# Kernel tuning notes

Measured on AMD Instinct MI355X. Metric: run time of the kernel, lower is better.

The kernel has to match this reference:

```python
import jax, jax.numpy as jnp
import numpy as np


def setup_inputs() -> dict:
    key = jax.random.key(0)
    ks = jax.random.split(key, 11)
    b, c, h, w = 16, 64, 16, 16
    F = 64  # num_filters
    O = 64  # num_outputs
    d_in = 2 * (c + 1)  # 130: concat of two (feature + coord) vectors
    s = 0.05
    return {
        "x_img": jax.random.normal(ks[0], (b, c, h, w), dtype=jnp.float32),
        "Wg0": jax.random.normal(ks[1], (F, d_in), dtype=jnp.float32) * s,
        "bg0": jax.random.normal(ks[2], (F,), dtype=jnp.float32) * s,
        "Wg1": jax.random.normal(ks[3], (F, F), dtype=jnp.float32) * s,
        "bg1": jax.random.normal(ks[4], (F,), dtype=jnp.float32) * s,
        "Wg2": jax.random.normal(ks[5], (F, F), dtype=jnp.float32) * s,
        "bg2": jax.random.normal(ks[6], (F,), dtype=jnp.float32) * s,
        "Wp": jax.random.normal(ks[7], (F, F), dtype=jnp.float32) * s,
        "bp": jax.random.normal(ks[8], (F,), dtype=jnp.float32) * s,
        "Wo": jax.random.normal(ks[9], (O, F), dtype=jnp.float32) * s,
        "bo": jax.random.normal(ks[10], (O,), dtype=jnp.float32) * s,
    }


def reference(x_img, Wg0, bg0, Wg1, bg1, Wg2, bg2, Wp, bp, Wo, bo):
    b, c, h, w = x_img.shape
    L = h * w
    # [b, L, c]: flatten spatial, move channels last
    feats = x_img.reshape(b, c, L).transpose(0, 2, 1)
    # append 1-d coordinate feature -> [b, L, c+1]
    coord = jnp.broadcast_to(
        jnp.arange(L, dtype=feats.dtype).reshape(1, L, 1), (b, L, 1)
    )
    feats = jnp.concatenate([feats, coord], axis=2)
    # pairwise broadcast-concat: pair[b, p, q] = [feats[b, q], feats[b, p]]
    d = feats.shape[-1]
    x_i = jnp.broadcast_to(feats[:, None, :, :], (b, L, L, d))
    x_j = jnp.broadcast_to(feats[:, :, None, :], (b, L, L, d))
    pair = jnp.concatenate([x_i, x_j], axis=3)  # [b, L, L, 2*(c+1)]
    # shared g-MLP (3 layers, ReLU)
    out = jax.nn.relu(jnp.einsum("bpqd,fd->bpqf", pair, Wg0) + bg0)
    out = jax.nn.relu(jnp.einsum("bpqf,gf->bpqg", out, Wg1) + bg1)
    out = jax.nn.relu(jnp.einsum("bpqf,gf->bpqg", out, Wg2) + bg2)
    # sum-reduce over both pair dims -> [b, F]
    out = out.sum(axis=(1, 2))
    # f-network
    out = jax.nn.relu(out @ Wp.T + bp)
    out = out @ Wo.T + bo
    return out
```

## Files before the change

### kernel.cpp

```cpp
#include <hip/hip_runtime.h>


typedef short s8v __attribute__((ext_vector_type(8)));
typedef short s4v __attribute__((ext_vector_type(4)));
typedef float f4v __attribute__((ext_vector_type(4)));

#define KEEP(x) asm volatile("" : "+v"(x))

#define MFMA16(a, b, c) __builtin_amdgcn_mfma_f32_16x16x16bf16_1k(a, b, c, 0, 0, 0)

__device__ __forceinline__ short bfr(float v) {
  return __builtin_bit_cast(short, (__bf16)v);
}
__device__ __forceinline__ f4v relu4(f4v v) {
  f4v z = {0.f, 0.f, 0.f, 0.f};
  return __builtin_elementwise_max(v, z);
}
__device__ __forceinline__ s8v cvt8(f4v a, f4v b) {
  s8v r;
  r[0] = bfr(a[0]); r[1] = bfr(a[1]); r[2] = bfr(a[2]); r[3] = bfr(a[3]);
  r[4] = bfr(b[0]); r[5] = bfr(b[1]); r[6] = bfr(b[2]); r[7] = bfr(b[3]);
  return r;
}
__device__ __forceinline__ s4v cvt4(f4v a) {
  s4v r;
  r[0] = bfr(a[0]); r[1] = bfr(a[1]); r[2] = bfr(a[2]); r[3] = bfr(a[3]);
  return r;
}
__device__ __forceinline__ f4v ldf4(const float* p) {
  return *(const f4v*)p;
}

__global__ __launch_bounds__(256) void k_pre(
    const float* __restrict__ x, const float* __restrict__ Wg0,
    const float* __restrict__ bg0, float* __restrict__ Ag,
    float* __restrict__ Bg) {
  __shared__ float ws[64 * 131];
  __shared__ float xs[64 * 17];

  const int t = threadIdx.x;
  const int b = blockIdx.x >> 4;
  const int l0 = (blockIdx.x & 15) * 16;

  for (int i = t; i < 64 * 130; i += 256) {
    int f = i / 130, d = i - f * 130;
    ws[f * 131 + d] = Wg0[i];
  }
  for (int i = t; i < 64 * 16; i += 256) {
    int ch = i >> 4, li = i & 15;
    xs[ch * 17 + li] = x[b * 16384 + ch * 256 + l0 + li];
  }
  __syncthreads();

  const int f = t & 63;
  const int w = t >> 6;
  float accA[4] = {0.f, 0.f, 0.f, 0.f};
  float accB[4] = {0.f, 0.f, 0.f, 0.f};
  for (int d = 0; d < 64; ++d) {
    float wa = ws[f * 131 + d];
    float wb = ws[f * 131 + 65 + d];
#pragma unroll
    for (int i = 0; i < 4; ++i) {
      float xv = xs[d * 17 + w + 4 * i];
      accA[i] += xv * wa;
      accB[i] += xv * wb;
    }
  }
  const float wca = ws[f * 131 + 64];
  const float wcb = ws[f * 131 + 129];
  const float bias = bg0[f];
#pragma unroll
  for (int i = 0; i < 4; ++i) {
    int l = l0 + w + 4 * i;
    Ag[(b * 256 + l) * 64 + f] = accA[i] + (float)l * wca;
    Bg[(b * 256 + l) * 64 + f] = accB[i] + (float)l * wcb + bias;
  }
}

__global__ __launch_bounds__(256, 1) void k_main(
    const float* __restrict__ Ag, const float* __restrict__ Bg,
    const float* __restrict__ Wg1, const float* __restrict__ bg1,
    const float* __restrict__ Wg2, const float* __restrict__ bg2,
    float* __restrict__ Part) {
  __shared__ __align__(16) float Bs[32 * 64];
  __shared__ float Sblk[64];

  const int t = threadIdx.x;
  const int wid = t >> 6;
  const int lane = t & 63;
  const int mm = lane & 15;
  const int quad = lane >> 4;
  const int b = blockIdx.y;
  const int blkx = blockIdx.x;
  const int qq = blkx & 3;
  const int p0 = (blkx >> 2) * 32;
  const int q0 = (qq * 4 + wid) * 16;

  if (t < 64) Sblk[t] = 0.f;

  {
    const f4v* Bb4 = (const f4v*)(Bg + (b * 256 + p0) * 64);
    ((f4v*)Bs)[t] = Bb4[t];
    ((f4v*)Bs)[t + 256] = Bb4[t + 256];
  }

  const float* Arow = Ag + (b * 256 + q0 + mm) * 64;
  f4v af0 = ldf4(Arow + quad * 8);
  f4v af1 = ldf4(Arow + quad * 8 + 4);
  f4v af2 = ldf4(Arow + 32 + quad * 8);
  f4v af3 = ldf4(Arow + 36 + quad * 8);

  s8v W1f[4][2];
  s4v W2f[4][4];
  f4v c1i[4], c2i[4];
#pragma unroll
  for (int gt = 0; gt < 4; ++gt) {
    c1i[gt] = ldf4(bg1 + gt * 16 + quad * 4);
    c2i[gt] = ldf4(bg2 + gt * 16 + quad * 4);
#pragma unroll
    for (int kh = 0; kh < 2; ++kh) {
      const float* r1 = Wg1 + (gt * 16 + mm) * 64 + kh * 32 + quad * 8;
      W1f[gt][kh] = cvt8(ldf4(r1), ldf4(r1 + 4));
    }
#pragma unroll
    for (int kt = 0; kt < 4; ++kt) {
      const float* r2 = Wg2 + (gt * 16 + mm) * 64 + kt * 16 + quad * 4;
      W2f[gt][kt] = cvt4(ldf4(r2));
    }
  }
#pragma unroll
  for (int gt = 0; gt < 4; ++gt) {
    KEEP(W1f[gt][0]); KEEP(W1f[gt][1]);
    KEEP(W2f[gt][0]); KEEP(W2f[gt][1]); KEEP(W2f[gt][2]); KEEP(W2f[gt][3]);
    KEEP(c1i[gt]); KEEP(c2i[gt]);
  }
  KEEP(af0); KEEP(af1); KEEP(af2); KEEP(af3);

  __syncthreads();

  f4v cs[4] = {{0.f,0.f,0.f,0.f},{0.f,0.f,0.f,0.f},
               {0.f,0.f,0.f,0.f},{0.f,0.f,0.f,0.f}};

  f4v bq0 = ldf4(Bs + quad * 8);
  f4v bq1 = ldf4(Bs + quad * 8 + 4);
  f4v bq2 = ldf4(Bs + 32 + quad * 8);
  f4v bq3 = ldf4(Bs + 36 + quad * 8);

  for (int ip = 0; ip < 32; ++ip) {
    const float* bn = Bs + ((ip < 31) ? ip + 1 : 31) * 64;
    f4v bn0 = ldf4(bn + quad * 8);
    f4v bn1 = ldf4(bn + quad * 8 + 4);
    f4v bn2 = ldf4(bn + 32 + quad * 8);
    f4v bn3 = ldf4(bn + 36 + quad * 8);

    s8v x0 = cvt8(relu4(af0 + bq0), relu4(af1 + bq1));
    s8v x1 = cvt8(relu4(af2 + bq2), relu4(af3 + bq3));

    s4v pk[4];
#pragma unroll
    for (int gt = 0; gt < 4; ++gt) {
      f4v a = c1i[gt];
      a = __builtin_amdgcn_mfma_f32_16x16x32_bf16(W1f[gt][0], x0, a, 0, 0, 0);
      a = __builtin_amdgcn_mfma_f32_16x16x32_bf16(W1f[gt][1], x1, a, 0, 0, 0);
      pk[gt] = cvt4(relu4(a));
    }
#pragma unroll
    for (int ot = 0; ot < 4; ++ot) {
      f4v a = c2i[ot];
      a = MFMA16(W2f[ot][0], pk[0], a);
      a = MFMA16(W2f[ot][1], pk[1], a);
      a = MFMA16(W2f[ot][2], pk[2], a);
      a = MFMA16(W2f[ot][3], pk[3], a);
      cs[ot] += relu4(a);
    }

    bq0 = bn0; bq1 = bn1; bq2 = bn2; bq3 = bn3;
  }

#pragma unroll
  for (int ot = 0; ot < 4; ++ot) {
#pragma unroll
    for (int r = 0; r < 4; ++r) {
      float v = cs[ot][r];
      v += __shfl_xor(v, 1);
      v += __shfl_xor(v, 2);
      v += __shfl_xor(v, 4);
      v += __shfl_xor(v, 8);
      if (mm == 0) atomicAdd(&Sblk[ot * 16 + quad * 4 + r], v);
    }
  }
  __syncthreads();
  if (t < 64) Part[(b * 32 + blkx) * 64 + t] = Sblk[t];
}

__global__ __launch_bounds__(64) void k_final(
    const float* __restrict__ Part, const float* __restrict__ Wp,
    const float* __restrict__ bp, const float* __restrict__ Wo,
    const float* __restrict__ bo, float* __restrict__ out) {
  __shared__ float sv[64], tv[64];
  const int b = blockIdx.x, t = threadIdx.x;
  float s = 0.f;
  const float* Pb = Part + b * 32 * 64;
#pragma unroll
  for (int j = 0; j < 32; ++j) s += Pb[j * 64 + t];
  sv[t] = s;
  __syncthreads();
  float acc = bp[t];
  for (int g = 0; g < 64; ++g) acc += sv[g] * Wp[t * 64 + g];
  tv[t] = fmaxf(acc, 0.f);
  __syncthreads();
  float o = bo[t];
  for (int f = 0; f < 64; ++f) o += tv[f] * Wo[t * 64 + f];
  out[b * 64 + t] = o;
}

extern "C" void kernel_launch(void* const* d_in, const int* in_sizes, int n_in,
                              void* d_out, int out_size, void* d_ws, size_t ws_size,
                              hipStream_t stream) {
  const float* x   = (const float*)d_in[0];
  const float* Wg0 = (const float*)d_in[1];
  const float* bg0 = (const float*)d_in[2];
  const float* Wg1 = (const float*)d_in[3];
  const float* bg1 = (const float*)d_in[4];
  const float* Wg2 = (const float*)d_in[5];
  const float* bg2 = (const float*)d_in[6];
  const float* Wp  = (const float*)d_in[7];
  const float* bp  = (const float*)d_in[8];
  const float* Wo  = (const float*)d_in[9];
  const float* bo  = (const float*)d_in[10];
  float* out = (float*)d_out;

  float* Ag   = (float*)d_ws;
  float* Bg   = Ag + 16 * 256 * 64;
  float* Part = Bg + 16 * 256 * 64;

  k_pre<<<256, 256, 0, stream>>>(x, Wg0, bg0, Ag, Bg);
  k_main<<<dim3(32, 16), 256, 0, stream>>>(Ag, Bg, Wg1, bg1, Wg2, bg2, Part);
  k_final<<<16, 64, 0, stream>>>(Part, Wp, bp, Wo, bo, out);
}
```

Baseline: 124.0 us.

## Halve per-block p-rows, double grid, raise occupancy, and use bit-trick bf16 packing

Each k_main block now covers 16 p-rows instead of 32, so the grid doubles to 64x16 blocks, and launch bounds ask for 3 blocks per CU. This is meant to fill more CUs and hide latency through occupancy. The float-to-bf16 conversion is replaced by an add-and-shift round-to-nearest packing of two values per 32-bit word, which is cheaper but does not handle NaN ties exactly. The manual prefetch of B rows is dropped for a partially unrolled loop, and k_final now reduces 64 partials per batch.

```diff
diff --git a/kernel.cpp b/kernel.cpp
--- a/kernel.cpp
+++ b/kernel.cpp
@@ -4,28 +4,30 @@
 typedef short s8v __attribute__((ext_vector_type(8)));
 typedef short s4v __attribute__((ext_vector_type(4)));
 typedef float f4v __attribute__((ext_vector_type(4)));
+typedef unsigned u4v __attribute__((ext_vector_type(4)));
+typedef unsigned u2v __attribute__((ext_vector_type(2)));
 
 #define KEEP(x) asm volatile("" : "+v"(x))
 
 #define MFMA16(a, b, c) __builtin_amdgcn_mfma_f32_16x16x16bf16_1k(a, b, c, 0, 0, 0)
 
-__device__ __forceinline__ short bfr(float v) {
-  return __builtin_bit_cast(short, (__bf16)v);
+__device__ __forceinline__ unsigned pkrh(float a, float b) {
+  unsigned ua = __builtin_bit_cast(unsigned, a) + 0x8000u;
+  unsigned ub = __builtin_bit_cast(unsigned, b) + 0x8000u;
+  return (ua >> 16) | (ub & 0xFFFF0000u);
 }
 __device__ __forceinline__ f4v relu4(f4v v) {
   f4v z = {0.f, 0.f, 0.f, 0.f};
   return __builtin_elementwise_max(v, z);
 }
 __device__ __forceinline__ s8v cvt8(f4v a, f4v b) {
-  s8v r;
-  r[0] = bfr(a[0]); r[1] = bfr(a[1]); r[2] = bfr(a[2]); r[3] = bfr(a[3]);
-  r[4] = bfr(b[0]); r[5] = bfr(b[1]); r[6] = bfr(b[2]); r[7] = bfr(b[3]);
-  return r;
+  u4v u = {pkrh(a[0], a[1]), pkrh(a[2], a[3]),
+           pkrh(b[0], b[1]), pkrh(b[2], b[3])};
+  return __builtin_bit_cast(s8v, u);
 }
 __device__ __forceinline__ s4v cvt4(f4v a) {
-  s4v r;
-  r[0] = bfr(a[0]); r[1] = bfr(a[1]); r[2] = bfr(a[2]); r[3] = bfr(a[3]);
-  return r;
+  u2v u = {pkrh(a[0], a[1]), pkrh(a[2], a[3])};
+  return __builtin_bit_cast(s4v, u);
 }
 __device__ __forceinline__ f4v ldf4(const float* p) {
   return *(const f4v*)p;
@@ -77,12 +79,12 @@
   }
 }
 
-__global__ __launch_bounds__(256, 1) void k_main(
+__global__ __launch_bounds__(256, 3) void k_main(
     const float* __restrict__ Ag, const float* __restrict__ Bg,
     const float* __restrict__ Wg1, const float* __restrict__ bg1,
     const float* __restrict__ Wg2, const float* __restrict__ bg2,
     float* __restrict__ Part) {
-  __shared__ __align__(16) float Bs[32 * 64];
+  __shared__ __align__(16) float Bs[16 * 64];
   __shared__ float Sblk[64];
 
   const int t = threadIdx.x;
@@ -93,7 +95,7 @@
   const int b = blockIdx.y;
   const int blkx = blockIdx.x;
   const int qq = blkx & 3;
-  const int p0 = (blkx >> 2) * 32;
+  const int p0 = (blkx >> 2) * 16;
   const int q0 = (qq * 4 + wid) * 16;
 
   if (t < 64) Sblk[t] = 0.f;
@@ -101,7 +103,6 @@
   {
     const f4v* Bb4 = (const f4v*)(Bg + (b * 256 + p0) * 64);
     ((f4v*)Bs)[t] = Bb4[t];
-    ((f4v*)Bs)[t + 256] = Bb4[t + 256];
   }
 
   const float* Arow = Ag + (b * 256 + q0 + mm) * 64;
@@ -141,17 +142,13 @@
   f4v cs[4] = {{0.f,0.f,0.f,0.f},{0.f,0.f,0.f,0.f},
                {0.f,0.f,0.f,0.f},{0.f,0.f,0.f,0.f}};
 
-  f4v bq0 = ldf4(Bs + quad * 8);
-  f4v bq1 = ldf4(Bs + quad * 8 + 4);
-  f4v bq2 = ldf4(Bs + 32 + quad * 8);
-  f4v bq3 = ldf4(Bs + 36 + quad * 8);
-
-  for (int ip = 0; ip < 32; ++ip) {
-    const float* bn = Bs + ((ip < 31) ? ip + 1 : 31) * 64;
-    f4v bn0 = ldf4(bn + quad * 8);
-    f4v bn1 = ldf4(bn + quad * 8 + 4);
-    f4v bn2 = ldf4(bn + 32 + quad * 8);
-    f4v bn3 = ldf4(bn + 36 + quad * 8);
+#pragma unroll 4
+  for (int ip = 0; ip < 16; ++ip) {
+    const float* brow = Bs + ip * 64;
+    f4v bq0 = ldf4(brow + quad * 8);
+    f4v bq1 = ldf4(brow + quad * 8 + 4);
+    f4v bq2 = ldf4(brow + 32 + quad * 8);
+    f4v bq3 = ldf4(brow + 36 + quad * 8);
 
     s8v x0 = cvt8(relu4(af0 + bq0), relu4(af1 + bq1));
     s8v x1 = cvt8(relu4(af2 + bq2), relu4(af3 + bq3));
@@ -173,8 +170,6 @@
       a = MFMA16(W2f[ot][3], pk[3], a);
       cs[ot] += relu4(a);
     }
-
-    bq0 = bn0; bq1 = bn1; bq2 = bn2; bq3 = bn3;
   }
 
 #pragma unroll
@@ -190,7 +185,7 @@
     }
   }
   __syncthreads();
-  if (t < 64) Part[(b * 32 + blkx) * 64 + t] = Sblk[t];
+  if (t < 64) Part[(b * 64 + blkx) * 64 + t] = Sblk[t];
 }
 
 __global__ __launch_bounds__(64) void k_final(
@@ -200,9 +195,9 @@
   __shared__ float sv[64], tv[64];
   const int b = blockIdx.x, t = threadIdx.x;
   float s = 0.f;
-  const float* Pb = Part + b * 32 * 64;
-#pragma unroll
-  for (int j = 0; j < 32; ++j) s += Pb[j * 64 + t];
+  const float* Pb = Part + b * 64 * 64;
+#pragma unroll
+  for (int j = 0; j < 64; ++j) s += Pb[j * 64 + t];
   sv[t] = s;
   __syncthreads();
   float acc = bp[t];
@@ -235,6 +230,6 @@
   float* Part = Bg + 16 * 256 * 64;
 
   k_pre<<<256, 256, 0, stream>>>(x, Wg0, bg0, Ag, Bg);
-  k_main<<<dim3(32, 16), 256, 0, stream>>>(Ag, Bg, Wg1, bg1, Wg2, bg2, Part);
+  k_main<<<dim3(64, 16), 256, 0, stream>>>(Ag, Bg, Wg1, bg1, Wg2, bg2, Part);
   k_final<<<16, 64, 0, stream>>>(Part, Wp, bp, Wo, bo, out);
 }
```

Result: slower. 128.6 us (+3.7%).
